# Optimization experiments

Hardware: AMD Instinct MI355X
Metric: run time of the kernel (lower is better)

Reference implementation:

```python
import jax, jax.numpy as jnp
import numpy as np

B, T, HID, NH = 2, 2048, 1024, 16
HD = HID // NH  # head_dim = 64
ROPE_BASE = 1000000.0


def _precompute_freqs(dim, end, rope_base):
    inv = 1.0 / (rope_base ** (np.arange(0, dim, 2)[: dim // 2].astype(np.float32) / dim))
    t = np.arange(end, dtype=np.float32)
    freqs = np.outer(t, inv).astype(np.float32)  # (end, dim//2)
    cos = np.concatenate([np.cos(freqs), np.cos(freqs)], axis=-1)
    sin = np.concatenate([np.sin(freqs), np.sin(freqs)], axis=-1)
    return jnp.asarray(cos), jnp.asarray(sin)


def setup_inputs() -> dict:
    key = jax.random.key(0)
    ks = jax.random.split(key, 5)
    x = jax.random.normal(ks[0], (B, T, HID), dtype=jnp.float32)
    s = 1.0 / np.sqrt(HID)
    Wq = jax.random.normal(ks[1], (HID, HID), dtype=jnp.float32) * s
    Wk = jax.random.normal(ks[2], (HID, HID), dtype=jnp.float32) * s
    Wv = jax.random.normal(ks[3], (HID, HID), dtype=jnp.float32) * s
    Wo = jax.random.normal(ks[4], (HID, HID), dtype=jnp.float32) * s
    cos, sin = _precompute_freqs(HD, T, ROPE_BASE)
    return {"x": x, "Wq": Wq, "Wk": Wk, "Wv": Wv, "Wo": Wo, "cos": cos, "sin": sin}


def _rotate_half(u):
    half = u.shape[-1] // 2
    return jnp.concatenate([-u[..., half:], u[..., :half]], axis=-1)


def reference(x, Wq, Wk, Wv, Wo, cos, sin):
    b, t, _ = x.shape
    # projections (nn.Linear: x @ W.T)
    q = (x @ Wq.T).reshape(b, t, NH, HD).transpose(0, 2, 1, 3)  # (B,H,T,D)
    k = (x @ Wk.T).reshape(b, t, NH, HD).transpose(0, 2, 1, 3)
    v = (x @ Wv.T).reshape(b, t, NH, HD).transpose(0, 2, 1, 3)
    c = cos[None, None, :t, :]
    s = sin[None, None, :t, :]
    q = q * c + _rotate_half(q) * s
    k = k * c + _rotate_half(k) * s
    scores = jnp.einsum("bhqd,bhkd->bhqk", q, k) / jnp.sqrt(jnp.float32(HD))
    causal = jnp.tril(jnp.ones((t, t), dtype=bool))
    scores = jnp.where(causal[None, None], scores, jnp.float32(-jnp.inf))
    prob = jax.nn.softmax(scores, axis=-1)
    out = jnp.einsum("bhqk,bhkd->bhqd", prob, v)
    out = out.transpose(0, 2, 1, 3).reshape(b, t, HID)
    return out @ Wo.T
```

## Files before the change

kernel.cpp:

```cpp
#include <hip/hip_runtime.h>
#include <hip/hip_bf16.h>

#define B_   2
#define T_   2048
#define HID_ 1024
#define NH_  16
#define HD_  64
#define K_   1024
#define M_   (B_*T_)

typedef __attribute__((ext_vector_type(8)))  short bf16x8;
typedef __attribute__((ext_vector_type(4)))  float f32x4;
typedef __attribute__((ext_vector_type(16))) float f32x16;
typedef __attribute__((ext_vector_type(4)))  unsigned int u32x4;
typedef __attribute__((ext_vector_type(2)))  unsigned int u32x2;

#define LOG2E 1.44269504088896340736f

__device__ inline unsigned short f2bf(float f) {
    __hip_bfloat16 h = __float2bfloat16(f);
    return __builtin_bit_cast(unsigned short, h);
}
__device__ inline unsigned int pk2(float a, float b) {
    return (unsigned int)f2bf(a) | ((unsigned int)f2bf(b) << 16);
}
__device__ inline unsigned int pkt(float a, float b) {
    return __builtin_amdgcn_perm(__builtin_bit_cast(unsigned, a),
                                 __builtin_bit_cast(unsigned, b), 0x03020706u);
}
__device__ inline bf16x8 cvt8(float4 a, float4 b) {
    bf16x8 r;
    r[0]=(short)f2bf(a.x); r[1]=(short)f2bf(a.y); r[2]=(short)f2bf(a.z); r[3]=(short)f2bf(a.w);
    r[4]=(short)f2bf(b.x); r[5]=(short)f2bf(b.y); r[6]=(short)f2bf(b.z); r[7]=(short)f2bf(b.w);
    return r;
}

__global__ __launch_bounds__(256)
void cast_all(const float* __restrict__ x,
              const float* __restrict__ W0, const float* __restrict__ W1,
              const float* __restrict__ W2, const float* __restrict__ W3,
              unsigned short* __restrict__ xo,
              unsigned short* __restrict__ o0, unsigned short* __restrict__ o1,
              unsigned short* __restrict__ o2, unsigned short* __restrict__ o3) {
    const int blk = blockIdx.x;
    const float* in;
    unsigned short* out;
    int i;
    if (blk < 2048) {
        in = x; out = xo; i = blk * 256 + threadIdx.x;
    } else {
        const int wb = blk - 2048, sec = wb >> 9;
        in  = (sec == 0) ? W0 : (sec == 1) ? W1 : (sec == 2) ? W2 : W3;
        out = (sec == 0) ? o0 : (sec == 1) ? o1 : (sec == 2) ? o2 : o3;
        i = (wb & 511) * 256 + threadIdx.x;
    }
    float4 a = ((const float4*)in)[2*i], b = ((const float4*)in)[2*i + 1];
    ((bf16x8*)out)[i] = cvt8(a, b);
}

template<int TYPE>
__global__ __launch_bounds__(256)
void gemm_k(const unsigned short* __restrict__ A, const unsigned short* __restrict__ W0,
            const unsigned short* __restrict__ W1, const unsigned short* __restrict__ W2,
            const float* __restrict__ cs, const float* __restrict__ sn,
            unsigned short* __restrict__ qb, unsigned short* __restrict__ kb,
            unsigned short* __restrict__ vtb, float* __restrict__ fout) {
    __shared__ unsigned short As[128*64];
    __shared__ unsigned short Bs[128*64];
    const int tid = threadIdx.x;
    const int w = tid >> 6, lane = tid & 63;
    const int u = lane >> 4, c = lane & 15;
    const int bid = blockIdx.x;
    const int xcd = bid & 7, idx = bid >> 3;
    int bmi, bni;
    if constexpr (TYPE == 0) {
        bmi = (xcd & 3) * 8 + (idx & 7);
        bni = (xcd >> 2) * 12 + (idx >> 3);
    } else {
        bmi = (xcd & 3) * 8 + (idx & 7);
        bni = (xcd >> 2) * 4 + (idx >> 3);
    }
    const int bm = bmi * 128, bn = bni * 128;
    const int wm = (w & 1) * 64, wn = (w >> 1) * 64;
    const int srow = tid >> 3, scol = (tid & 7) << 3;

    const unsigned short* Wsec;
    int wrowbase;
    if constexpr (TYPE == 0) {
        const int sec = bn >> 10;
        Wsec = (sec == 0) ? W0 : ((sec == 1) ? W1 : W2);
        wrowbase = bn & 1023;
    } else {
        Wsec = W0;
        wrowbase = bn;
    }
    const unsigned short* Wp = Wsec + (size_t)(wrowbase + srow) * K_ + scol;
    const unsigned short* Ap = A + (size_t)(bm + srow) * K_ + scol;

    f32x4 acc[4][4] = {};
    bf16x8 ra[4], rb[4];

    auto loadin = [&](int k0) {
        #pragma unroll
        for (int i = 0; i < 4; ++i) {
            ra[i] = *(const bf16x8*)(Ap + (size_t)i * 32 * K_ + k0);
            rb[i] = *(const bf16x8*)(Wp + (size_t)i * 32 * K_ + k0);
        }
    };
    loadin(0);

    for (int k0 = 0; k0 < K_; k0 += 64) {
        __syncthreads();
        #pragma unroll
        for (int i = 0; i < 4; ++i) {
            const int row = i * 32 + srow;
            const int sc = (scol * 2) ^ ((row & 7) << 4);
            *(bf16x8*)((char*)As + row * 128 + sc) = ra[i];
            *(bf16x8*)((char*)Bs + row * 128 + sc) = rb[i];
        }
        __syncthreads();
        if (k0 < K_ - 64) loadin(k0 + 64);
        #pragma unroll
        for (int kk = 0; kk < 2; ++kk) {
            bf16x8 af[4], bfr[4];
            #pragma unroll
            for (int mi = 0; mi < 4; ++mi) {
                const int row = wm + mi * 16 + c;
                const int sc = (kk * 64 + u * 16) ^ ((row & 7) << 4);
                af[mi] = *(const bf16x8*)((char*)As + row * 128 + sc);
            }
            #pragma unroll
            for (int ni = 0; ni < 4; ++ni) {
                const int row = wn + ni * 16 + c;
                const int sc = (kk * 64 + u * 16) ^ ((row & 7) << 4);
                bfr[ni] = *(const bf16x8*)((char*)Bs + row * 128 + sc);
            }
            #pragma unroll
            for (int mi = 0; mi < 4; ++mi)
                #pragma unroll
                for (int ni = 0; ni < 4; ++ni)
                    acc[mi][ni] = __builtin_amdgcn_mfma_f32_16x16x32_bf16(
                        af[mi], bfr[ni], acc[mi][ni], 0, 0, 0);
        }
    }

    if constexpr (TYPE == 1) {
        #pragma unroll
        for (int mi = 0; mi < 4; ++mi)
            #pragma unroll
            for (int ni = 0; ni < 4; ++ni)
                #pragma unroll
                for (int r = 0; r < 4; ++r)
                    fout[(size_t)(bm + wm + 16*mi + 4*u + r) * HID_ + (bn + wn + 16*ni + c)] =
                        acc[mi][ni][r];
    } else {
        const int sec = bn >> 10;
        const int h = ((bn + wn) & 1023) >> 6;
        if (sec == 2) {
            #pragma unroll
            for (int mi = 0; mi < 4; ++mi)
                #pragma unroll
                for (int r = 0; r < 4; ++r) {
                    const int mg = bm + wm + 16*mi + 4*u + r;
                    const int bb = mg >> 11, t = mg & 2047;
                    const int tk = (t & ~12) | ((t & 4) << 1) | ((t & 8) >> 1);
                    #pragma unroll
                    for (int ni = 0; ni < 4; ++ni)
                        vtb[((size_t)(bb*16 + h) * 64 + 16*ni + c) * 2048 + tk] =
                            f2bf(acc[mi][ni][r]);
                }
        } else {
            unsigned short* ob = sec ? kb : qb;
            const float qsc = sec ? 1.0f : (0.125f * LOG2E);
            #pragma unroll
            for (int mi = 0; mi < 4; ++mi)
                #pragma unroll
                for (int r = 0; r < 4; ++r) {
                    const int mg = bm + wm + 16*mi + 4*u + r;
                    const int bb = mg >> 11, t = mg & 2047;
                    const size_t base = ((size_t)(bb*16 + h) * 2048 + t) * 64;
                    #pragma unroll
                    for (int ni = 0; ni < 2; ++ni) {
                        const int dlo = 16*ni + c;
                        const float cv = cs[t*64 + dlo], sv = sn[t*64 + dlo];
                        const float Aa = acc[mi][ni][r], Bb = acc[mi][ni+2][r];
                        ob[base + dlo]      = f2bf((Aa*cv - Bb*sv) * qsc);
                        ob[base + dlo + 32] = f2bf((Bb*cv + Aa*sv) * qsc);
                    }
                }
        }
    }
}

__global__ __launch_bounds__(256)
void attn16(const unsigned short* __restrict__ q, const unsigned short* __restrict__ k,
            const unsigned short* __restrict__ vt, unsigned short* __restrict__ ab) {
    const int raw = blockIdx.x;
    const int bh     = (raw & 7) + 8 * ((raw >> 3) & 3);
    const int qchunk = 31 - (raw >> 5);
    const int tid = threadIdx.x;
    const int wid = tid >> 6, lane = tid & 63;
    const int h = lane >> 5, c = lane & 31;
    const int b = bh >> 4, hh = bh & 15;
    const int q0 = qchunk * 64;
    const int qgcA = q0 + c, qgcB = q0 + 32 + c;
    const int stAd = 2 * qchunk;
    const int NT   = 2 * qchunk + 2;
    const unsigned short* qp = q  + (size_t)bh * (T_*64);
    const unsigned short* kp = k  + (size_t)bh * (T_*64);
    const unsigned short* vp = vt + (size_t)bh * (64*T_);

    const int kloff  = c * 64 + 8 * h;
    const int vloff0 = c * 2048 + 8 * h;
    const int vloff1 = vloff0 + 32 * 2048;

    bf16x8 qfA[4], qfB[4];
    {
        const unsigned short* qrowA = qp + (q0 + c) * 64 + 8 * h;
        const unsigned short* qrowB = qrowA + 32 * 64;
        #pragma unroll
        for (int s = 0; s < 4; ++s) {
            qfA[s] = *(const bf16x8*)(qrowA + s * 16);
            qfB[s] = *(const bf16x8*)(qrowB + s * 16);
        }
    }

    f32x16 OA0 = {}, OA1 = {}, OB0 = {}, OB1 = {};
    float mA = -1e30f, lA = 0.f, mB = -1e30f, lB = 0.f;

    auto loadK = [&](bf16x8 (&kf)[4], int st) {
        const unsigned short* kst = kp + (st << 11);
        #pragma unroll
        for (int s = 0; s < 4; ++s)
            kf[s] = *(const bf16x8*)(kst + kloff + s * 16);
    };

    auto process = [&](bf16x8 (&kf)[4], int st) {
        const int kvs = st << 5;
        const unsigned short* vst = vp + (st << 5);
        bf16x8 vf0 = *(const bf16x8*)(vst + vloff0);
        bf16x8 vf1 = *(const bf16x8*)(vst + vloff0 + 16);
        bf16x8 vf2 = *(const bf16x8*)(vst + vloff1);
        bf16x8 vf3 = *(const bf16x8*)(vst + vloff1 + 16);
        const bool doA = (st <= stAd);
        float pA[16], pB[16];
        float mxA = -1e30f, mxB;
        if (doA) {
            __builtin_amdgcn_s_setprio(1);
            f32x16 sa = {};
            #pragma unroll
            for (int s = 0; s < 4; ++s)
                sa = __builtin_amdgcn_mfma_f32_32x32x16_bf16(kf[s], qfA[s], sa, 0, 0, 0);
            __builtin_amdgcn_s_setprio(0);
            #pragma unroll
            for (int r = 0; r < 16; ++r) pA[r] = sa[r];
            if (st == stAd) {
                #pragma unroll
                for (int r = 0; r < 16; ++r) {
                    const int kk = kvs + (r & 3) + 8 * (r >> 2) + 4 * h;
                    if (kk > qgcA) pA[r] = -1e30f;
                }
            }
            const float a0 = fmaxf(fmaxf(pA[0],  pA[1]),  pA[2]);
            const float a1 = fmaxf(fmaxf(pA[3],  pA[4]),  pA[5]);
            const float a2 = fmaxf(fmaxf(pA[6],  pA[7]),  pA[8]);
            const float a3 = fmaxf(fmaxf(pA[9],  pA[10]), pA[11]);
            const float a4 = fmaxf(fmaxf(pA[12], pA[13]), pA[14]);
            mxA = fmaxf(fmaxf(fmaxf(a0, a1), fmaxf(a2, a3)), fmaxf(a4, pA[15]));
        }
        {
            __builtin_amdgcn_s_setprio(1);
            f32x16 sa = {};
            #pragma unroll
            for (int s = 0; s < 4; ++s)
                sa = __builtin_amdgcn_mfma_f32_32x32x16_bf16(kf[s], qfB[s], sa, 0, 0, 0);
            __builtin_amdgcn_s_setprio(0);
            #pragma unroll
            for (int r = 0; r < 16; ++r) pB[r] = sa[r];
            if (st == NT - 1) {
                #pragma unroll
                for (int r = 0; r < 16; ++r) {
                    const int kk = kvs + (r & 3) + 8 * (r >> 2) + 4 * h;
                    if (kk > qgcB) pB[r] = -1e30f;
                }
            }
            const float a0 = fmaxf(fmaxf(pB[0],  pB[1]),  pB[2]);
            const float a1 = fmaxf(fmaxf(pB[3],  pB[4]),  pB[5]);
            const float a2 = fmaxf(fmaxf(pB[6],  pB[7]),  pB[8]);
            const float a3 = fmaxf(fmaxf(pB[9],  pB[10]), pB[11]);
            const float a4 = fmaxf(fmaxf(pB[12], pB[13]), pB[14]);
            mxB = fmaxf(fmaxf(fmaxf(a0, a1), fmaxf(a2, a3)), fmaxf(a4, pB[15]));
        }
        if (st + 4 < NT) loadK(kf, st + 4);
        if (!__all(fmaxf(mxA - mA, mxB - mB) <= 8.0f)) {
            if (doA) {
                const float fx = fmaxf(mxA, __shfl_xor(mxA, 32));
                const float mn = fmaxf(mA, fx);
                const float f = __builtin_amdgcn_exp2f(mA - mn);
                mA = mn; lA *= f;
                #pragma unroll
                for (int r = 0; r < 16; ++r) { OA0[r] *= f; OA1[r] *= f; }
            }
            {
                const float fx = fmaxf(mxB, __shfl_xor(mxB, 32));
                const float mn = fmaxf(mB, fx);
                const float f = __builtin_amdgcn_exp2f(mB - mn);
                mB = mn; lB *= f;
                #pragma unroll
                for (int r = 0; r < 16; ++r) { OB0[r] *= f; OB1[r] *= f; }
            }
        }
        if (doA) {
            float ps = 0.f;
            #pragma unroll
            for (int r = 0; r < 16; ++r) {
                pA[r] = __builtin_amdgcn_exp2f(pA[r] - mA);
                ps += pA[r];
            }
            lA += ps;
            u32x4 B0w = { pkt(pA[0],  pA[1]),  pkt(pA[2],  pA[3]),
                          pkt(pA[4],  pA[5]),  pkt(pA[6],  pA[7])  };
            u32x4 B1w = { pkt(pA[8],  pA[9]),  pkt(pA[10], pA[11]),
                          pkt(pA[12], pA[13]), pkt(pA[14], pA[15]) };
            bf16x8 PB0 = __builtin_bit_cast(bf16x8, B0w);
            bf16x8 PB1 = __builtin_bit_cast(bf16x8, B1w);
            __builtin_amdgcn_s_setprio(1);
            OA0 = __builtin_amdgcn_mfma_f32_32x32x16_bf16(vf0, PB0, OA0, 0, 0, 0);
            OA0 = __builtin_amdgcn_mfma_f32_32x32x16_bf16(vf1, PB1, OA0, 0, 0, 0);
            OA1 = __builtin_amdgcn_mfma_f32_32x32x16_bf16(vf2, PB0, OA1, 0, 0, 0);
            OA1 = __builtin_amdgcn_mfma_f32_32x32x16_bf16(vf3, PB1, OA1, 0, 0, 0);
            __builtin_amdgcn_s_setprio(0);
        }
        {
            float ps = 0.f;
            #pragma unroll
            for (int r = 0; r < 16; ++r) {
                pB[r] = __builtin_amdgcn_exp2f(pB[r] - mB);
                ps += pB[r];
            }
            lB += ps;
            u32x4 B0w = { pkt(pB[0],  pB[1]),  pkt(pB[2],  pB[3]),
                          pkt(pB[4],  pB[5]),  pkt(pB[6],  pB[7])  };
            u32x4 B1w = { pkt(pB[8],  pB[9]),  pkt(pB[10], pB[11]),
                          pkt(pB[12], pB[13]), pkt(pB[14], pB[15]) };
            bf16x8 PB0 = __builtin_bit_cast(bf16x8, B0w);
            bf16x8 PB1 = __builtin_bit_cast(bf16x8, B1w);
            __builtin_amdgcn_s_setprio(1);
            OB0 = __builtin_amdgcn_mfma_f32_32x32x16_bf16(vf0, PB0, OB0, 0, 0, 0);
            OB0 = __builtin_amdgcn_mfma_f32_32x32x16_bf16(vf1, PB1, OB0, 0, 0, 0);
            OB1 = __builtin_amdgcn_mfma_f32_32x32x16_bf16(vf2, PB0, OB1, 0, 0, 0);
            OB1 = __builtin_amdgcn_mfma_f32_32x32x16_bf16(vf3, PB1, OB1, 0, 0, 0);
            __builtin_amdgcn_s_setprio(0);
        }
    };

    bf16x8 kf_[4];
    if (wid < NT) {
        loadK(kf_, wid);
        for (int st = wid; st < NT; st += 4)
            process(kf_, st);
    }
    lA += __shfl_xor(lA, 32);
    lB += __shfl_xor(lB, 32);

    __shared__ unsigned OSu[4][64 * 34];
    __shared__ float mS[4][64], lS[4][64];
    if (h == 0) {
        mS[wid][c] = mA;      lS[wid][c] = lA;
        mS[wid][32 + c] = mB; lS[wid][32 + c] = lB;
    }
    {
        unsigned* os = &OSu[wid][0];
        const int rbA = c * 34 + 2 * h;
        const int rbB = (32 + c) * 34 + 2 * h;
        #pragma unroll
        for (int j = 0; j < 4; ++j) {
            os[rbA + 4*j]          = pk2(OA0[4*j],   OA0[4*j+1]);
            os[rbA + 4*j + 1]      = pk2(OA0[4*j+2], OA0[4*j+3]);
            os[rbA + 16 + 4*j]     = pk2(OA1[4*j],   OA1[4*j+1]);
            os[rbA + 16 + 4*j + 1] = pk2(OA1[4*j+2], OA1[4*j+3]);
            os[rbB + 4*j]          = pk2(OB0[4*j],   OB0[4*j+1]);
            os[rbB + 4*j + 1]      = pk2(OB0[4*j+2], OB0[4*j+3]);
            os[rbB + 16 + 4*j]     = pk2(OB1[4*j],   OB1[4*j+1]);
            os[rbB + 16 + 4*j + 1] = pk2(OB1[4*j+2], OB1[4*j+3]);
        }
    }
    __syncthreads();

    const int ql = tid & 63, ug = (tid >> 6) * 8;
    const float M = fmaxf(fmaxf(mS[0][ql], mS[1][ql]), fmaxf(mS[2][ql], mS[3][ql]));
    float acc[16] = {};
    float L = 0.f;
    #pragma unroll
    for (int w2 = 0; w2 < 4; ++w2) {
        const float sc = __builtin_amdgcn_exp2f(mS[w2][ql] - M);
        L += lS[w2][ql] * sc;
        u32x4 pa = *(u32x4*)&OSu[w2][ql * 34 + ug];
        u32x4 pb = *(u32x4*)&OSu[w2][ql * 34 + ug + 4];
        #pragma unroll
        for (int t = 0; t < 4; ++t) {
            acc[2*t]     += __builtin_bit_cast(float, pa[t] << 16) * sc;
            acc[2*t+1]   += __builtin_bit_cast(float, pa[t] & 0xffff0000u) * sc;
            acc[8+2*t]   += __builtin_bit_cast(float, pb[t] << 16) * sc;
            acc[8+2*t+1] += __builtin_bit_cast(float, pb[t] & 0xffff0000u) * sc;
        }
    }
    const float inv = 1.0f / L;
    uint4 ov0, ov1;
    ov0.x = pk2(acc[0]*inv,  acc[1]*inv);
    ov0.y = pk2(acc[2]*inv,  acc[3]*inv);
    ov0.z = pk2(acc[4]*inv,  acc[5]*inv);
    ov0.w = pk2(acc[6]*inv,  acc[7]*inv);
    ov1.x = pk2(acc[8]*inv,  acc[9]*inv);
    ov1.y = pk2(acc[10]*inv, acc[11]*inv);
    ov1.z = pk2(acc[12]*inv, acc[13]*inv);
    ov1.w = pk2(acc[14]*inv, acc[15]*inv);
    unsigned short* orow = ab + ((size_t)(b * T_) + q0 + ql) * HID_ + hh * 64 + ug * 2;
    *(uint4*)orow       = ov0;
    *(uint4*)(orow + 8) = ov1;
}

extern "C" void kernel_launch(void* const* d_in, const int* in_sizes, int n_in,
                              void* d_out, int out_size, void* d_ws, size_t ws_size,
                              hipStream_t stream) {
    const float* x  = (const float*)d_in[0];
    const float* Wq = (const float*)d_in[1];
    const float* Wk = (const float*)d_in[2];
    const float* Wv = (const float*)d_in[3];
    const float* Wo = (const float*)d_in[4];
    const float* cs = (const float*)d_in[5];
    const float* sn = (const float*)d_in[6];
    char* wsb = (char*)d_ws;
    unsigned short* xb  = (unsigned short*)(wsb);
    unsigned short* wqb = (unsigned short*)(wsb + (8u  << 20));
    unsigned short* wkb = (unsigned short*)(wsb + (10u << 20));
    unsigned short* wvb = (unsigned short*)(wsb + (12u << 20));
    unsigned short* wob = (unsigned short*)(wsb + (14u << 20));
    unsigned short* qb  = (unsigned short*)(wsb + (16u << 20));
    unsigned short* kb  = (unsigned short*)(wsb + (24u << 20));
    unsigned short* vtb = (unsigned short*)(wsb + (32u << 20));
    unsigned short* ab  = (unsigned short*)(wsb + (40u << 20));

    cast_all<<<4096, 256, 0, stream>>>(x, Wq, Wk, Wv, Wo, xb, wqb, wkb, wvb, wob);

    gemm_k<0><<<768, 256, 0, stream>>>(
        xb, wqb, wkb, wvb, cs, sn, qb, kb, vtb, nullptr);
    attn16<<<1024, 256, 0, stream>>>(qb, kb, vtb, ab);
    gemm_k<1><<<256, 256, 0, stream>>>(
        ab, wob, nullptr, nullptr, nullptr, nullptr,
        nullptr, nullptr, nullptr, (float*)d_out);
}
```

Baseline: 117.2 us.

## Stream GEMM tiles straight into double-buffered LDS via global_load_lds

Replaces the register-staged global-to-LDS copy in the projection GEMM with direct global_load_lds (16-byte) transfers into a double-buffered LDS tile, prefetching the next K slice while the current one feeds MFMA. This drops the register round trip and one barrier per iteration and doubles LDS use per block. It also drops the XOR swizzle, so fragment reads from the row-major 128-byte-stride tiles may hit LDS bank conflicts. There is no explicit vmcnt wait before the barrier, so correctness relies on the compiler inserting one.

```diff
diff --git a/kernel.cpp b/kernel.cpp
--- a/kernel.cpp
+++ b/kernel.cpp
@@ -33,6 +33,11 @@
     r[0]=(short)f2bf(a.x); r[1]=(short)f2bf(a.y); r[2]=(short)f2bf(a.z); r[3]=(short)f2bf(a.w);
     r[4]=(short)f2bf(b.x); r[5]=(short)f2bf(b.y); r[6]=(short)f2bf(b.z); r[7]=(short)f2bf(b.w);
     return r;
+}
+__device__ inline void gll16(const void* g, void* l) {
+    __builtin_amdgcn_global_load_lds(
+        (const __attribute__((address_space(1))) unsigned int*)g,
+        (__attribute__((address_space(3))) unsigned int*)l, 16, 0, 0);
 }
 
 __global__ __launch_bounds__(256)
@@ -65,8 +70,8 @@
             const float* __restrict__ cs, const float* __restrict__ sn,
             unsigned short* __restrict__ qb, unsigned short* __restrict__ kb,
             unsigned short* __restrict__ vtb, float* __restrict__ fout) {
-    __shared__ unsigned short As[128*64];
-    __shared__ unsigned short Bs[128*64];
+    __shared__ unsigned short As[2][128*64];
+    __shared__ unsigned short Bs[2][128*64];
     const int tid = threadIdx.x;
     const int w = tid >> 6, lane = tid & 63;
     const int u = lane >> 4, c = lane & 15;
@@ -82,7 +87,6 @@
     }
     const int bm = bmi * 128, bn = bni * 128;
     const int wm = (w & 1) * 64, wn = (w >> 1) * 64;
-    const int srow = tid >> 3, scol = (tid & 7) << 3;
 
     const unsigned short* Wsec;
     int wrowbase;
@@ -94,47 +98,38 @@
         Wsec = W0;
         wrowbase = bn;
     }
-    const unsigned short* Wp = Wsec + (size_t)(wrowbase + srow) * K_ + scol;
-    const unsigned short* Ap = A + (size_t)(bm + srow) * K_ + scol;
+    const unsigned short* Ab = A + (size_t)bm * K_;
+    const unsigned short* Wb = Wsec + (size_t)wrowbase * K_;
+    const int srow = lane >> 3;
+    const int scol = (lane & 7) * 8;
 
     f32x4 acc[4][4] = {};
-    bf16x8 ra[4], rb[4];
-
-    auto loadin = [&](int k0) {
-        #pragma unroll
-        for (int i = 0; i < 4; ++i) {
-            ra[i] = *(const bf16x8*)(Ap + (size_t)i * 32 * K_ + k0);
-            rb[i] = *(const bf16x8*)(Wp + (size_t)i * 32 * K_ + k0);
+
+    auto stage = [&](int buf, int k0) {
+        #pragma unroll
+        for (int s4 = 0; s4 < 4; ++s4) {
+            const int seg = w * 4 + s4;
+            gll16(Ab + (size_t)(seg * 8 + srow) * K_ + k0 + scol,
+                  (char*)&As[buf][0] + seg * 1024);
+            gll16(Wb + (size_t)(seg * 8 + srow) * K_ + k0 + scol,
+                  (char*)&Bs[buf][0] + seg * 1024);
         }
     };
-    loadin(0);
-
+
+    stage(0, 0);
+    __syncthreads();
+    int cur = 0;
     for (int k0 = 0; k0 < K_; k0 += 64) {
-        __syncthreads();
-        #pragma unroll
-        for (int i = 0; i < 4; ++i) {
-            const int row = i * 32 + srow;
-            const int sc = (scol * 2) ^ ((row & 7) << 4);
-            *(bf16x8*)((char*)As + row * 128 + sc) = ra[i];
-            *(bf16x8*)((char*)Bs + row * 128 + sc) = rb[i];
-        }
-        __syncthreads();
-        if (k0 < K_ - 64) loadin(k0 + 64);
+        if (k0 + 64 < K_) stage(cur ^ 1, k0 + 64);
         #pragma unroll
         for (int kk = 0; kk < 2; ++kk) {
             bf16x8 af[4], bfr[4];
             #pragma unroll
-            for (int mi = 0; mi < 4; ++mi) {
-                const int row = wm + mi * 16 + c;
-                const int sc = (kk * 64 + u * 16) ^ ((row & 7) << 4);
-                af[mi] = *(const bf16x8*)((char*)As + row * 128 + sc);
-            }
-            #pragma unroll
-            for (int ni = 0; ni < 4; ++ni) {
-                const int row = wn + ni * 16 + c;
-                const int sc = (kk * 64 + u * 16) ^ ((row & 7) << 4);
-                bfr[ni] = *(const bf16x8*)((char*)Bs + row * 128 + sc);
-            }
+            for (int mi = 0; mi < 4; ++mi)
+                af[mi] = *(const bf16x8*)&As[cur][(wm + mi*16 + c) * 64 + kk*32 + u*8];
+            #pragma unroll
+            for (int ni = 0; ni < 4; ++ni)
+                bfr[ni] = *(const bf16x8*)&Bs[cur][(wn + ni*16 + c) * 64 + kk*32 + u*8];
             #pragma unroll
             for (int mi = 0; mi < 4; ++mi)
                 #pragma unroll
@@ -142,6 +137,8 @@
                     acc[mi][ni] = __builtin_amdgcn_mfma_f32_16x16x32_bf16(
                         af[mi], bfr[ni], acc[mi][ni], 0, 0, 0);
         }
+        __syncthreads();
+        cur ^= 1;
     }
 
     if constexpr (TYPE == 1) {
```

New measurement: 142.7 us. 21.7% more time.
